# Kernel optimization log

Measured on AMD Instinct MI355X. Metric: run time of the kernel, lower is better.

## Reference

```python
import jax, jax.numpy as jnp
import numpy as np

N_HEADS = 16
ROPE_BASE = 10000.0


def _rope_tables(T, head_dim, dtype):
    d2 = head_dim // 2
    inv_freq = 1.0 / (ROPE_BASE ** (jnp.arange(0, head_dim, 2, dtype=jnp.float32) / head_dim))
    t = jnp.arange(T, dtype=jnp.float32)
    freqs = jnp.outer(t, inv_freq)  # [T, d2]
    cos = jnp.cos(freqs)[None, :, None, :].astype(dtype)  # [1,T,1,d2]
    sin = jnp.sin(freqs)[None, :, None, :].astype(dtype)
    return cos, sin


def _apply_rotary(x, cos, sin):
    # x: [B,T,H,D]; rotate halves
    d = x.shape[-1] // 2
    x1, x2 = x[..., :d], x[..., d:]
    return jnp.concatenate([x1 * cos + x2 * sin, -x1 * sin + x2 * cos], axis=-1)


def setup_inputs() -> dict:
    key = jax.random.key(0)
    k1, k2, k3 = jax.random.split(key, 3)
    B, T, C = 2, 2048, 1024
    x = jax.random.normal(k1, (B, T, C), dtype=jnp.float32)
    w_attn = jax.random.normal(k2, (3 * C, C), dtype=jnp.float32) * (1.0 / np.sqrt(C))
    w_proj = jax.random.normal(k3, (C, C), dtype=jnp.float32) * (1.0 / np.sqrt(C))
    return {"x": x, "w_attn": w_attn, "w_proj": w_proj}


def reference(x, w_attn, w_proj):
    B, T, C = x.shape
    H = N_HEADS
    D = C // H
    qkv = jnp.einsum('btc,fc->btf', x, w_attn)  # [B,T,3C]
    q, k, v = jnp.split(qkv, 3, axis=2)
    q = q.reshape(B, T, H, D)
    k = k.reshape(B, T, H, D)
    v = v.reshape(B, T, H, D)
    cos, sin = _rope_tables(T, D, x.dtype)
    q = _apply_rotary(q, cos, sin)
    k = _apply_rotary(k, cos, sin)
    # causal SDPA, scale 1/sqrt(D)
    scale = 1.0 / np.sqrt(D)
    scores = jnp.einsum('bqhd,bkhd->bhqk', q, k) * scale
    causal = jnp.tril(jnp.ones((T, T), dtype=bool))
    scores = jnp.where(causal[None, None], scores, jnp.finfo(scores.dtype).min)
    attn = jax.nn.softmax(scores, axis=-1)
    y = jnp.einsum('bhqk,bkhd->bqhd', attn, v).reshape(B, T, C)
    return jnp.einsum('btc,oc->bto', y, w_proj)
```

## Files before the change

kernel.cpp:

```cpp
#include <hip/hip_runtime.h>
#include <math.h>

typedef __bf16 bf16x8 __attribute__((ext_vector_type(8)));
typedef float f32x4 __attribute__((ext_vector_type(4)));

__device__ __forceinline__ unsigned f2bf(float f) {
    union { float f; unsigned u; } v; v.f = f;
    return (v.u + 0x7FFFu + ((v.u >> 16) & 1u)) >> 16;
}

__device__ __forceinline__ unsigned cvtpk(float a, float b) {
    unsigned r;
    __asm__("v_cvt_pk_bf16_f32 %0, %1, %2" : "=v"(r) : "v"(a), "v"(b));
    return r;
}

__device__ __forceinline__ void gload16(const ushort* g, ushort* l) {
    __builtin_amdgcn_global_load_lds(
        (const __attribute__((address_space(1))) void*)g,
        (__attribute__((address_space(3))) void*)l, 16, 0, 0);
}

__device__ __forceinline__ bool src_is_fp32(const unsigned* s) {
    int sane = 0;
#pragma unroll
    for (int i = 0; i < 64; ++i) {
        unsigned lo = s[i] & 0xFFFFu;
        unsigned e = (lo >> 7) & 0xFF;
        if (lo == 0u || (e >= 100u && e <= 140u)) sane++;
    }
    return sane < 48;
}

__global__ __launch_bounds__(256) void tobf16_all_kernel(
    const unsigned* __restrict__ s0, const unsigned* __restrict__ s1,
    const unsigned* __restrict__ s2,
    ushort* __restrict__ d0, ushort* __restrict__ d1, ushort* __restrict__ d2) {
    const int bx = blockIdx.x;
    const unsigned* src;
    ushort* dst;
    int lb;
    if (bx < 2048)      { src = s0; dst = d0; lb = bx; }
    else if (bx < 3584) { src = s1; dst = d1; lb = bx - 2048; }
    else                { src = s2; dst = d2; lb = bx - 3584; }
    const int i = lb * 2048 + threadIdx.x * 8;
    if (src_is_fp32(src)) {
        const float* fs = (const float*)src;
        float4 f0 = *(const float4*)(fs + i);
        float4 f1 = *(const float4*)(fs + i + 4);
        uint4 o;
        o.x = f2bf(f0.x) | (f2bf(f0.y) << 16);
        o.y = f2bf(f0.z) | (f2bf(f0.w) << 16);
        o.z = f2bf(f1.x) | (f2bf(f1.y) << 16);
        o.w = f2bf(f1.z) | (f2bf(f1.w) << 16);
        *(uint4*)(dst + i) = o;
    } else {
        *(uint4*)(dst + i) = *(const uint4*)((const ushort*)src + i);
    }
}

constexpr int GBM = 128, GBN = 128, GBK = 32;

__global__ __launch_bounds__(256) void gemm_qkv_rope_kernel(
    const ushort* __restrict__ A, const ushort* __restrict__ Bmat,
    ushort* __restrict__ qkvh, int K) {
    __shared__ ushort As[2][GBM * GBK];
    __shared__ ushort Bs[2][GBN * GBK];

    const int tid  = threadIdx.x;
    const int lane = tid & 63;
    const int wv   = tid >> 6;
    const int wm   = (wv >> 1) * 64;
    const int wn   = (wv & 1) * 64;

    const ushort* Ab = A + (size_t)blockIdx.x * GBM * K;
    const ushort* Bb = Bmat + (size_t)blockIdx.y * GBN * K;

    f32x4 acc[4][4];
#pragma unroll
    for (int i = 0; i < 4; i++)
#pragma unroll
        for (int j = 0; j < 4; j++) acc[i][j] = (f32x4){0.f, 0.f, 0.f, 0.f};

    const int srow = tid >> 2;
    const int scol = (tid & 3) * 8;
    const int fr = lane & 15;
    const int fk = (lane >> 4) * 8;
    const int nK = K >> 5;

    gload16(Ab + (size_t)srow * K + scol,        As[0] + wv * 512);
    gload16(Ab + (size_t)(srow + 64) * K + scol, As[0] + wv * 512 + 2048);
    gload16(Bb + (size_t)srow * K + scol,        Bs[0] + wv * 512);
    gload16(Bb + (size_t)(srow + 64) * K + scol, Bs[0] + wv * 512 + 2048);

#pragma unroll 1
    for (int it = 0; it < nK; ++it) {
        const int cur = it & 1;
        __syncthreads();
        if (it + 1 < nK) {
            const int k0 = (it + 1) << 5, nxt = cur ^ 1;
            gload16(Ab + (size_t)srow * K + k0 + scol,        As[nxt] + wv * 512);
            gload16(Ab + (size_t)(srow + 64) * K + k0 + scol, As[nxt] + wv * 512 + 2048);
            gload16(Bb + (size_t)srow * K + k0 + scol,        Bs[nxt] + wv * 512);
            gload16(Bb + (size_t)(srow + 64) * K + k0 + scol, Bs[nxt] + wv * 512 + 2048);
        }
        bf16x8 af[4], bfr[4];
#pragma unroll
        for (int i = 0; i < 4; i++)
            af[i] = *(const bf16x8*)(As[cur] + (wm + i * 16 + fr) * GBK + fk);
#pragma unroll
        for (int j = 0; j < 4; j++)
            bfr[j] = *(const bf16x8*)(Bs[cur] + (wn + j * 16 + fr) * GBK + fk);
#pragma unroll
        for (int i = 0; i < 4; i++)
#pragma unroll
            for (int j = 0; j < 4; j++)
                acc[i][j] = __builtin_amdgcn_mfma_f32_16x16x32_bf16(af[i], bfr[j], acc[i][j], 0, 0, 0);
    }

    const int crow0 = (lane >> 4) * 4;
    const int col0  = blockIdx.y * GBN + wn;
    const int which = col0 >> 10;
    const int hh    = (col0 >> 6) & 15;
    ushort* outp = qkvh + (size_t)which * 4194304 + (size_t)hh * 131072;

    if (which < 2) {
        const float inva = exp2f((float)fr * -0.41524101186f);
        const float invb = exp2f((float)(fr + 16) * -0.41524101186f);
        const float qs = (which == 0) ? 0.125f : 1.0f;
#pragma unroll
        for (int i = 0; i < 4; i++)
#pragma unroll
            for (int r = 0; r < 4; r++) {
                int row = blockIdx.x * GBM + wm + i * 16 + crow0 + r;
                int t = row & 2047;
                size_t ob = ((size_t)(row >> 11)) * 2097152 + (size_t)t * 64;
                float sa, ca, sb, cb;
                __sincosf((float)t * inva, &sa, &ca);
                __sincosf((float)t * invb, &sb, &cb);
                float q0 = acc[i][0][r], q1 = acc[i][1][r];
                float q2 = acc[i][2][r], q3 = acc[i][3][r];
                float n0 = (q0 * ca + q2 * sa) * qs;
                float n1 = (q1 * cb + q3 * sb) * qs;
                float n2 = (q2 * ca - q0 * sa) * qs;
                float n3 = (q3 * cb - q1 * sb) * qs;
                unsigned u01 = cvtpk(n0, n1);
                unsigned u23 = cvtpk(n2, n3);
                outp[ob + fr]      = (ushort)(u01 & 0xFFFFu);
                outp[ob + 16 + fr] = (ushort)(u01 >> 16);
                outp[ob + 32 + fr] = (ushort)(u23 & 0xFFFFu);
                outp[ob + 48 + fr] = (ushort)(u23 >> 16);
            }
    } else {
#pragma unroll
        for (int i = 0; i < 4; i++)
#pragma unroll
            for (int r = 0; r < 4; r++) {
                int row = blockIdx.x * GBM + wm + i * 16 + crow0 + r;
                int t = row & 2047;
                size_t ob = ((size_t)(row >> 11)) * 2097152 + (size_t)t * 64;
                unsigned u01 = cvtpk(acc[i][0][r], acc[i][1][r]);
                unsigned u23 = cvtpk(acc[i][2][r], acc[i][3][r]);
                outp[ob + fr]      = (ushort)(u01 & 0xFFFFu);
                outp[ob + 16 + fr] = (ushort)(u01 >> 16);
                outp[ob + 32 + fr] = (ushort)(u23 & 0xFFFFu);
                outp[ob + 48 + fr] = (ushort)(u23 >> 16);
            }
    }
}

__global__ __launch_bounds__(256) void gemm_bt_kernel(
    const ushort* __restrict__ A, const ushort* __restrict__ Bmat,
    float* __restrict__ C, int M, int N, int K) {
    __shared__ ushort As[2][GBM * GBK];
    __shared__ ushort Bs[2][GBN * GBK];

    const int tid  = threadIdx.x;
    const int lane = tid & 63;
    const int wv   = tid >> 6;
    const int wm   = (wv >> 1) * 64;
    const int wn   = (wv & 1) * 64;

    const ushort* Ab = A + (size_t)blockIdx.x * GBM * K;
    const ushort* Bb = Bmat + (size_t)blockIdx.y * GBN * K;

    f32x4 acc[4][4];
#pragma unroll
    for (int i = 0; i < 4; i++)
#pragma unroll
        for (int j = 0; j < 4; j++) acc[i][j] = (f32x4){0.f, 0.f, 0.f, 0.f};

    const int srow = tid >> 2;
    const int scol = (tid & 3) * 8;
    const int fr = lane & 15;
    const int fk = (lane >> 4) * 8;
    const int nK = K >> 5;

    gload16(Ab + (size_t)srow * K + scol,        As[0] + wv * 512);
    gload16(Ab + (size_t)(srow + 64) * K + scol, As[0] + wv * 512 + 2048);
    gload16(Bb + (size_t)srow * K + scol,        Bs[0] + wv * 512);
    gload16(Bb + (size_t)(srow + 64) * K + scol, Bs[0] + wv * 512 + 2048);

#pragma unroll 1
    for (int it = 0; it < nK; ++it) {
        const int cur = it & 1;
        __syncthreads();
        if (it + 1 < nK) {
            const int k0 = (it + 1) << 5, nxt = cur ^ 1;
            gload16(Ab + (size_t)srow * K + k0 + scol,        As[nxt] + wv * 512);
            gload16(Ab + (size_t)(srow + 64) * K + k0 + scol, As[nxt] + wv * 512 + 2048);
            gload16(Bb + (size_t)srow * K + k0 + scol,        Bs[nxt] + wv * 512);
            gload16(Bb + (size_t)(srow + 64) * K + k0 + scol, Bs[nxt] + wv * 512 + 2048);
        }
        bf16x8 af[4], bfr[4];
#pragma unroll
        for (int i = 0; i < 4; i++)
            af[i] = *(const bf16x8*)(As[cur] + (wm + i * 16 + fr) * GBK + fk);
#pragma unroll
        for (int j = 0; j < 4; j++)
            bfr[j] = *(const bf16x8*)(Bs[cur] + (wn + j * 16 + fr) * GBK + fk);
#pragma unroll
        for (int i = 0; i < 4; i++)
#pragma unroll
            for (int j = 0; j < 4; j++)
                acc[i][j] = __builtin_amdgcn_mfma_f32_16x16x32_bf16(af[i], bfr[j], acc[i][j], 0, 0, 0);
    }

    const int crow0 = (lane >> 4) * 4;
#pragma unroll
    for (int i = 0; i < 4; i++)
#pragma unroll
        for (int j = 0; j < 4; j++)
#pragma unroll
            for (int r = 0; r < 4; r++) {
                int row = blockIdx.x * GBM + wm + i * 16 + crow0 + r;
                int col = blockIdx.y * GBN + wn + j * 16 + fr;
                C[(size_t)row * N + col] = acc[i][j][r];
            }
}

#define NEG_BIG (-1e30f)
constexpr int LPK = 72;
constexpr int LPV = 136;

__global__ __launch_bounds__(1024) void attn_kernel(const ushort* __restrict__ qkvh,
                                                    ushort* __restrict__ y) {
    __shared__ ushort Ks[2][128 * LPK];
    __shared__ ushort Vt[2][64 * LPV];
    __shared__ ushort Ps[16][16 * LPK];

    const int tid  = threadIdx.x;
    const int lane = tid & 63;
    const int wv   = tid >> 6;
    const int half = wv >> 3;
    const int wq   = wv & 7;
    const int jb   = half * 4;
    const int pid  = blockIdx.x;
    const int bh   = blockIdx.y;
    const int b    = bh >> 4, h = bh & 15;

    const ushort* qp = qkvh + (size_t)b * 2097152 + (size_t)h * 131072;
    const ushort* kp = qp + 4194304;
    const ushort* vp = qp + 8388608;

    const int fr = lane & 15;
    const int fq = lane >> 4;
    const int fk = fq * 8;

    const int srow = tid >> 3;
    const int scol = (tid & 7) * 8;
    const int vkey = tid & 127;
    const int vd0  = (tid >> 7) * 8;

#pragma unroll 1
    for (int seg = 0; seg < 2; ++seg) {
        const int qb = seg ? (15 - pid) : pid;
        const int nIt = qb + 1;

        __syncthreads();

        const int qrow = qb * 128 + wq * 16 + fr;
        bf16x8 qf0 = *(const bf16x8*)(qp + (size_t)qrow * 64 + fk);
        bf16x8 qf1 = *(const bf16x8*)(qp + (size_t)qrow * 64 + 32 + fk);

        f32x4 o[4];
        o[0] = o[1] = o[2] = o[3] = (f32x4){0.f, 0.f, 0.f, 0.f};
        float lacc[4] = {0.f, 0.f, 0.f, 0.f};

        uint4 kr, vr;
        {
            kr = *(const uint4*)(kp + (size_t)srow * 64 + scol);
            vr = *(const uint4*)(vp + (size_t)vkey * 64 + vd0);
            *(uint4*)(Ks[0] + srow * LPK + scol) = kr;
            unsigned w[4] = {vr.x, vr.y, vr.z, vr.w};
#pragma unroll
            for (int t = 0; t < 4; ++t) {
                Vt[0][(vd0 + 2 * t)     * LPV + vkey] = (ushort)(w[t] & 0xFFFFu);
                Vt[0][(vd0 + 2 * t + 1) * LPV + vkey] = (ushort)(w[t] >> 16);
            }
        }
        if (1 < nIt) {
            kr = *(const uint4*)(kp + (size_t)(128 + srow) * 64 + scol);
            vr = *(const uint4*)(vp + (size_t)(128 + vkey) * 64 + vd0);
        }

#pragma unroll 1
        for (int it = 0; it < nIt; ++it) {
            const int cur = it & 1;
            const int k0 = it * 128;
            __syncthreads();
            if (it + 1 < nIt) {
                const int nxt = cur ^ 1;
                *(uint4*)(Ks[nxt] + srow * LPK + scol) = kr;
                unsigned w[4] = {vr.x, vr.y, vr.z, vr.w};
#pragma unroll
                for (int t = 0; t < 4; ++t) {
                    Vt[nxt][(vd0 + 2 * t)     * LPV + vkey] = (ushort)(w[t] & 0xFFFFu);
                    Vt[nxt][(vd0 + 2 * t + 1) * LPV + vkey] = (ushort)(w[t] >> 16);
                }
                if (it + 2 < nIt) {
                    kr = *(const uint4*)(kp + (size_t)(k0 + 256 + srow) * 64 + scol);
                    vr = *(const uint4*)(vp + (size_t)(k0 + 256 + vkey) * 64 + vd0);
                }
            }

            f32x4 s[4];
#pragma unroll
            for (int jl = 0; jl < 4; ++jl) {
                const int j = jb + jl;
                bf16x8 kf0 = *(const bf16x8*)(Ks[cur] + (j * 16 + fr) * LPK + fk);
                bf16x8 kf1 = *(const bf16x8*)(Ks[cur] + (j * 16 + fr) * LPK + 32 + fk);
                f32x4 z = (f32x4){0.f, 0.f, 0.f, 0.f};
                z = __builtin_amdgcn_mfma_f32_16x16x32_bf16(qf0, kf0, z, 0, 0, 0);
                z = __builtin_amdgcn_mfma_f32_16x16x32_bf16(qf1, kf1, z, 0, 0, 0);
                s[jl] = z;
            }
            if (it + 1 < nIt) {
#pragma unroll
                for (int jl = 0; jl < 4; ++jl)
#pragma unroll
                    for (int r = 0; r < 4; ++r) {
                        float p = __expf(s[jl][r]);
                        s[jl][r] = p;
                        lacc[r] += p;
                    }
            } else {
                const int rowg = qb * 128 + wq * 16 + fq * 4;
#pragma unroll
                for (int jl = 0; jl < 4; ++jl)
#pragma unroll
                    for (int r = 0; r < 4; ++r) {
                        float v = s[jl][r];
                        if ((k0 + (jb + jl) * 16 + fr) > (rowg + r)) v = NEG_BIG;
                        float p = __expf(v);
                        s[jl][r] = p;
                        lacc[r] += p;
                    }
            }

            ushort* pw = Ps[wv];
#pragma unroll
            for (int jl = 0; jl < 4; jl += 2)
#pragma unroll
                for (int r = 0; r < 4; ++r) {
                    unsigned u = cvtpk(s[jl][r], s[jl + 1][r]);
                    pw[(fq * 4 + r) * LPK + jl * 16 + fr]       = (ushort)(u & 0xFFFFu);
                    pw[(fq * 4 + r) * LPK + (jl + 1) * 16 + fr] = (ushort)(u >> 16);
                }
            __asm__ volatile("" ::: "memory");

#pragma unroll
            for (int kl = 0; kl < 2; ++kl) {
                bf16x8 pf = *(const bf16x8*)(pw + fr * LPK + kl * 32 + fk);
                const int vcol = half * 64 + kl * 32 + fk;
#pragma unroll
                for (int j4 = 0; j4 < 4; ++j4) {
                    bf16x8 vf = *(const bf16x8*)(Vt[cur] + (j4 * 16 + fr) * LPV + vcol);
                    o[j4] = __builtin_amdgcn_mfma_f32_16x16x32_bf16(pf, vf, o[j4], 0, 0, 0);
                }
            }
        }

#pragma unroll
        for (int msk = 1; msk < 16; msk <<= 1)
#pragma unroll
            for (int r = 0; r < 4; ++r)
                lacc[r] += __shfl_xor(lacc[r], msk, 64);

        __syncthreads();
        float* ex = (float*)(&Ks[0][0]) + wq * 1104;
        if (half) {
#pragma unroll
            for (int j4 = 0; j4 < 4; ++j4)
#pragma unroll
                for (int r = 0; r < 4; ++r)
                    ex[lane * 17 + j4 * 4 + r] = o[j4][r];
#pragma unroll
            for (int r = 0; r < 4; ++r)
                ex[1088 + fq * 4 + r] = lacc[r];
        }
        __syncthreads();
        if (!half) {
            float linv[4];
#pragma unroll
            for (int r = 0; r < 4; ++r)
                linv[r] = 1.0f / (lacc[r] + ex[1088 + fq * 4 + r]);
#pragma unroll
            for (int j4 = 0; j4 < 4; j4 += 2)
#pragma unroll
                for (int r = 0; r < 4; ++r) {
                    int row = qb * 128 + wq * 16 + fq * 4 + r;
                    size_t yb = ((size_t)b * 2048 + row) * 1024 + h * 64;
                    float v0 = (o[j4][r]     + ex[lane * 17 + j4 * 4 + r])     * linv[r];
                    float v1 = (o[j4 + 1][r] + ex[lane * 17 + (j4 + 1) * 4 + r]) * linv[r];
                    unsigned u = cvtpk(v0, v1);
                    y[yb + j4 * 16 + fr]       = (ushort)(u & 0xFFFFu);
                    y[yb + (j4 + 1) * 16 + fr] = (ushort)(u >> 16);
                }
        }
    }
}

extern "C" void kernel_launch(void* const* d_in, const int* in_sizes, int n_in,
                              void* d_out, int out_size, void* d_ws, size_t ws_size,
                              hipStream_t stream) {
    const int nx = in_sizes[0];
    const int na = in_sizes[1];
    const int np = in_sizes[2];

    ushort* qkvh = (ushort*)d_ws;
    ushort* yb   = qkvh + (size_t)3 * 4194304;
    ushort* xb   = yb + (size_t)4096 * 1024;
    ushort* wab  = xb + nx;
    ushort* wpb  = wab + na;
    size_t need = ((size_t)3 * 4194304 + (size_t)4096 * 1024 + nx + na + np) * 2;
    if (ws_size < need) return;

    tobf16_all_kernel<<<dim3(4096), 256, 0, stream>>>(
        (const unsigned*)d_in[0], (const unsigned*)d_in[1], (const unsigned*)d_in[2],
        xb, wab, wpb);

    gemm_qkv_rope_kernel<<<dim3(32, 24), 256, 0, stream>>>(xb, wab, qkvh, 1024);
    attn_kernel<<<dim3(8, 32), 1024, 0, stream>>>(qkvh, yb);
    gemm_bt_kernel<<<dim3(32, 8), 256, 0, stream>>>(yb, wpb, (float*)d_out, 4096, 1024, 1024);
}
```

Measured before the change: 188.6 us.

## Compute transposed QK^T and build P operand via lane shuffles instead of LDS

Swaps the MFMA operand order so the score tile comes out transposed, with each lane holding one query row's values across keys. The P fragment for the PV MFMA is then assembled in registers through ds_bpermute-style shuffles rather than written to and read back from a per-wave LDS scratch buffer. Row sums collapse to one scalar per lane with two xor-shuffles. This removes the Ps shared array and its LDS round trip, freeing shared memory. In exchange it adds 16 cross-lane shuffles per iteration plus select logic, and the causal mask indexing changes with the new layout.

```diff
diff --git a/kernel.cpp b/kernel.cpp
--- a/kernel.cpp
+++ b/kernel.cpp
@@ -247,7 +247,6 @@
                                                     ushort* __restrict__ y) {
     __shared__ ushort Ks[2][128 * LPK];
     __shared__ ushort Vt[2][64 * LPV];
-    __shared__ ushort Ps[16][16 * LPK];
 
     const int tid  = threadIdx.x;
     const int lane = tid & 63;
@@ -272,6 +271,10 @@
     const int vkey = tid & 127;
     const int vd0  = (tid >> 7) * 8;
 
+    const int slA = fr + 32 * (fq & 1);
+    const int slB = slA + 16;
+    const bool hi = (fq >> 1) != 0;
+
 #pragma unroll 1
     for (int seg = 0; seg < 2; ++seg) {
         const int qb = seg ? (15 - pid) : pid;
@@ -285,7 +288,7 @@
 
         f32x4 o[4];
         o[0] = o[1] = o[2] = o[3] = (f32x4){0.f, 0.f, 0.f, 0.f};
-        float lacc[4] = {0.f, 0.f, 0.f, 0.f};
+        float lsum = 0.f;
 
         uint4 kr, vr;
         {
@@ -331,8 +334,8 @@
                 bf16x8 kf0 = *(const bf16x8*)(Ks[cur] + (j * 16 + fr) * LPK + fk);
                 bf16x8 kf1 = *(const bf16x8*)(Ks[cur] + (j * 16 + fr) * LPK + 32 + fk);
                 f32x4 z = (f32x4){0.f, 0.f, 0.f, 0.f};
-                z = __builtin_amdgcn_mfma_f32_16x16x32_bf16(qf0, kf0, z, 0, 0, 0);
-                z = __builtin_amdgcn_mfma_f32_16x16x32_bf16(qf1, kf1, z, 0, 0, 0);
+                z = __builtin_amdgcn_mfma_f32_16x16x32_bf16(kf0, qf0, z, 0, 0, 0);
+                z = __builtin_amdgcn_mfma_f32_16x16x32_bf16(kf1, qf1, z, 0, 0, 0);
                 s[jl] = z;
             }
             if (it + 1 < nIt) {
@@ -342,50 +345,54 @@
                     for (int r = 0; r < 4; ++r) {
                         float p = __expf(s[jl][r]);
                         s[jl][r] = p;
-                        lacc[r] += p;
+                        lsum += p;
                     }
             } else {
-                const int rowg = qb * 128 + wq * 16 + fq * 4;
 #pragma unroll
                 for (int jl = 0; jl < 4; ++jl)
 #pragma unroll
                     for (int r = 0; r < 4; ++r) {
                         float v = s[jl][r];
-                        if ((k0 + (jb + jl) * 16 + fr) > (rowg + r)) v = NEG_BIG;
+                        if ((k0 + (jb + jl) * 16 + fq * 4 + r) > qrow) v = NEG_BIG;
                         float p = __expf(v);
                         s[jl][r] = p;
-                        lacc[r] += p;
+                        lsum += p;
                     }
             }
 
-            ushort* pw = Ps[wv];
-#pragma unroll
-            for (int jl = 0; jl < 4; jl += 2)
-#pragma unroll
-                for (int r = 0; r < 4; ++r) {
-                    unsigned u = cvtpk(s[jl][r], s[jl + 1][r]);
-                    pw[(fq * 4 + r) * LPK + jl * 16 + fr]       = (ushort)(u & 0xFFFFu);
-                    pw[(fq * 4 + r) * LPK + (jl + 1) * 16 + fr] = (ushort)(u >> 16);
-                }
-            __asm__ volatile("" ::: "memory");
+            unsigned u0[4], u1[4];
+#pragma unroll
+            for (int jl = 0; jl < 4; ++jl) {
+                u0[jl] = cvtpk(s[jl][0], s[jl][1]);
+                u1[jl] = cvtpk(s[jl][2], s[jl][3]);
+            }
+            unsigned A0[4], A1[4], B0[4], B1[4];
+#pragma unroll
+            for (int jl = 0; jl < 4; ++jl) {
+                A0[jl] = __shfl(u0[jl], slA, 64);
+                A1[jl] = __shfl(u1[jl], slA, 64);
+                B0[jl] = __shfl(u0[jl], slB, 64);
+                B1[jl] = __shfl(u1[jl], slB, 64);
+            }
 
 #pragma unroll
             for (int kl = 0; kl < 2; ++kl) {
-                bf16x8 pf = *(const bf16x8*)(pw + fr * LPK + kl * 32 + fk);
+                union { unsigned u[4]; bf16x8 v; } pa;
+                pa.u[0] = hi ? A0[2 * kl + 1] : A0[2 * kl];
+                pa.u[1] = hi ? A1[2 * kl + 1] : A1[2 * kl];
+                pa.u[2] = hi ? B0[2 * kl + 1] : B0[2 * kl];
+                pa.u[3] = hi ? B1[2 * kl + 1] : B1[2 * kl];
                 const int vcol = half * 64 + kl * 32 + fk;
 #pragma unroll
                 for (int j4 = 0; j4 < 4; ++j4) {
                     bf16x8 vf = *(const bf16x8*)(Vt[cur] + (j4 * 16 + fr) * LPV + vcol);
-                    o[j4] = __builtin_amdgcn_mfma_f32_16x16x32_bf16(pf, vf, o[j4], 0, 0, 0);
+                    o[j4] = __builtin_amdgcn_mfma_f32_16x16x32_bf16(pa.v, vf, o[j4], 0, 0, 0);
                 }
             }
         }
 
-#pragma unroll
-        for (int msk = 1; msk < 16; msk <<= 1)
-#pragma unroll
-            for (int r = 0; r < 4; ++r)
-                lacc[r] += __shfl_xor(lacc[r], msk, 64);
+        lsum += __shfl_xor(lsum, 16, 64);
+        lsum += __shfl_xor(lsum, 32, 64);
 
         __syncthreads();
         float* ex = (float*)(&Ks[0][0]) + wq * 1104;
@@ -395,23 +402,23 @@
 #pragma unroll
                 for (int r = 0; r < 4; ++r)
                     ex[lane * 17 + j4 * 4 + r] = o[j4][r];
-#pragma unroll
-            for (int r = 0; r < 4; ++r)
-                ex[1088 + fq * 4 + r] = lacc[r];
+            if (fq == 0) ex[1088 + fr] = lsum;
         }
         __syncthreads();
         if (!half) {
             float linv[4];
 #pragma unroll
-            for (int r = 0; r < 4; ++r)
-                linv[r] = 1.0f / (lacc[r] + ex[1088 + fq * 4 + r]);
+            for (int r = 0; r < 4; ++r) {
+                float own = __shfl(lsum, fq * 4 + r, 64);
+                linv[r] = 1.0f / (own + ex[1088 + fq * 4 + r]);
+            }
 #pragma unroll
             for (int j4 = 0; j4 < 4; j4 += 2)
 #pragma unroll
                 for (int r = 0; r < 4; ++r) {
                     int row = qb * 128 + wq * 16 + fq * 4 + r;
                     size_t yb = ((size_t)b * 2048 + row) * 1024 + h * 64;
-                    float v0 = (o[j4][r]     + ex[lane * 17 + j4 * 4 + r])     * linv[r];
+                    float v0 = (o[j4][r]     + ex[lane * 17 + j4 * 4 + r])       * linv[r];
                     float v1 = (o[j4 + 1][r] + ex[lane * 17 + (j4 + 1) * 4 + r]) * linv[r];
                     unsigned u = cvtpk(v0, v1);
                     y[yb + j4 * 16 + fr]       = (ushort)(u & 0xFFFFu);
```

Measured after the change: 190.5 us. Within noise of the previous version (+1.0%).
